# Optimization experiments

Measured on AMD Instinct MI355X. Metric: run time of the kernel, lower is better.

## Reference

```python
import jax, jax.numpy as jnp
import numpy as np

GROUP_SIZE = 128
EPS = 1e-6
# AWQ nibble interleave order within each int32
_AWQ_SHIFTS = jnp.array([0, 4, 1, 5, 2, 6, 3, 7], dtype=jnp.uint32) * 4


def dequant_awq(qw, qz, sc, group_size=GROUP_SIZE):
    # qw: (in, out//8) int32, qz: (in//g, out//8) int32, sc: (in//g, out) float
    in_dim = qw.shape[0]
    w4 = ((qw.astype(jnp.uint32)[:, :, None] >> _AWQ_SHIFTS) & 0xF).astype(sc.dtype)
    z4 = ((qz.astype(jnp.uint32)[:, :, None] >> _AWQ_SHIFTS) & 0xF).astype(sc.dtype)
    w4 = w4.reshape(in_dim, -1)                    # (in, out)
    z4 = z4.reshape(qz.shape[0], -1)               # (in//g, out)
    z = jnp.repeat(z4, group_size, axis=0)         # (in, out)
    s = jnp.repeat(sc, group_size, axis=0)         # (in, out)
    return (w4 - z) * s


def rmsnorm(x, w, eps=EPS):
    return x * w * jax.lax.rsqrt(jnp.mean(x * x, axis=-1, keepdims=True) + eps)


def setup_inputs() -> dict:
    key = jax.random.key(0)
    ks = jax.random.split(key, 16)
    H, I, G = 2048, 8192, GROUP_SIZE
    IMAX = 2**31 - 1
    d = {}
    d['x'] = jax.random.normal(ks[0], (2, 2048, H), dtype=jnp.float32)
    d['ln1_w'] = jnp.ones((H,), jnp.float32)
    d['ln2_w'] = jnp.ones((H,), jnp.float32)
    d['qkv_qw'] = jax.random.randint(ks[1], (H, 3 * H // 8), 0, IMAX, dtype=jnp.int32)
    d['qkv_qz'] = jax.random.randint(ks[2], (H // G, 3 * H // 8), 0, IMAX, dtype=jnp.int32)
    d['qkv_sc'] = jax.random.normal(ks[3], (H // G, 3 * H), dtype=jnp.float32) * 0.02
    d['o_qw'] = jax.random.randint(ks[4], (H, H // 8), 0, IMAX, dtype=jnp.int32)
    d['o_qz'] = jax.random.randint(ks[5], (H // G, H // 8), 0, IMAX, dtype=jnp.int32)
    d['o_sc'] = jax.random.normal(ks[6], (H // G, H), dtype=jnp.float32) * 0.02
    d['gu_qw'] = jax.random.randint(ks[7], (H, 2 * I // 8), 0, IMAX, dtype=jnp.int32)
    d['gu_qz'] = jax.random.randint(ks[8], (H // G, 2 * I // 8), 0, IMAX, dtype=jnp.int32)
    d['gu_sc'] = jax.random.normal(ks[9], (H // G, 2 * I), dtype=jnp.float32) * 0.02
    d['dn_qw'] = jax.random.randint(ks[10], (I, H // 8), 0, IMAX, dtype=jnp.int32)
    d['dn_qz'] = jax.random.randint(ks[11], (I // G, H // 8), 0, IMAX, dtype=jnp.int32)
    d['dn_sc'] = jax.random.normal(ks[12], (I // G, H), dtype=jnp.float32) * 0.02
    return d


def reference(x, ln1_w, ln2_w, qkv_qw, qkv_qz, qkv_sc, o_qw, o_qz, o_sc,
              gu_qw, gu_qz, gu_sc, dn_qw, dn_qz, dn_sc):
    H = x.shape[-1]
    # attention-ish block (mock: qkv proj, take q slice, o proj)
    residual = x
    h = rmsnorm(x, ln1_w)
    qkv = h @ dequant_awq(qkv_qw, qkv_qz, qkv_sc)          # (..., 3H)
    q = qkv[..., :H]
    o = q @ dequant_awq(o_qw, o_qz, o_sc)                  # (..., H)
    x = residual + o
    # SwiGLU MLP
    residual = x
    h = rmsnorm(x, ln2_w)
    gate_up = h @ dequant_awq(gu_qw, gu_qz, gu_sc)         # (..., 2I)
    gate, up = jnp.split(gate_up, 2, axis=-1)
    mlp = (jax.nn.silu(gate) * up) @ dequant_awq(dn_qw, dn_qz, dn_sc)
    return residual + mlp
```

## Files before the change

### kernel.cpp

```cpp
#include <hip/hip_runtime.h>
#include <hip/hip_bf16.h>
#include <stdint.h>

typedef __bf16 bf16x8 __attribute__((ext_vector_type(8)));
typedef __bf16 bf16x2 __attribute__((ext_vector_type(2)));
typedef float  f32x4  __attribute__((ext_vector_type(4)));

template <int V> struct ic { static constexpr int value = V; };

__device__ __forceinline__ void gload_lds16(const void* g, void* l) {
  __builtin_amdgcn_global_load_lds(
      (const __attribute__((address_space(1))) void*)g,
      (__attribute__((address_space(3))) void*)l, 16, 0, 0);
}

__global__ __launch_bounds__(256) void rmsnorm_kernel(
    const float* __restrict__ x, const float* __restrict__ w,
    __bf16* __restrict__ out) {
  constexpr int H = 2048;
  const int row = blockIdx.x;
  const int t = threadIdx.x;
  const float4* xr = (const float4*)(x + (size_t)row * H);
  float4 a = xr[t * 2 + 0];
  float4 b = xr[t * 2 + 1];
  float ss = a.x*a.x + a.y*a.y + a.z*a.z + a.w*a.w
           + b.x*b.x + b.y*b.y + b.z*b.z + b.w*b.w;
#pragma unroll
  for (int o = 32; o > 0; o >>= 1) ss += __shfl_xor(ss, o);
  __shared__ float red[4];
  if ((t & 63) == 0) red[t >> 6] = ss;
  __syncthreads();
  float tot = red[0] + red[1] + red[2] + red[3];
  float r = rsqrtf(tot * (1.0f / H) + 1e-6f);
  const float4* wr4 = (const float4*)w;
  float4 wa = wr4[t * 2 + 0];
  float4 wb = wr4[t * 2 + 1];
  bf16x8 ov;
  ov[0] = (__bf16)(a.x * wa.x * r);
  ov[1] = (__bf16)(a.y * wa.y * r);
  ov[2] = (__bf16)(a.z * wa.z * r);
  ov[3] = (__bf16)(a.w * wa.w * r);
  ov[4] = (__bf16)(b.x * wb.x * r);
  ov[5] = (__bf16)(b.y * wb.y * r);
  ov[6] = (__bf16)(b.z * wb.z * r);
  ov[7] = (__bf16)(b.w * wb.w * r);
  *(bf16x8*)(out + (size_t)row * H + (size_t)t * 8) = ov;
}

template <int GU>
__global__ __launch_bounds__(256) void dequant_t_kernel(
    const int* __restrict__ qw, const int* __restrict__ qz,
    const float* __restrict__ sc, __bf16* __restrict__ wt,
    int K, int Cp, int Nfull) {
  const int t = threadIdx.x;
  const int k0 = blockIdx.x * 128 + (t & 63) * 2;
  const int c0 = blockIdx.y * 64 + (t >> 6) * 16;
  const int g = k0 >> 7;
  const uint32_t* qw0 = (const uint32_t*)qw + (size_t)k0 * Cp + c0;
  const uint32_t* qw1 = qw0 + Cp;
  const uint32_t* qzr = (const uint32_t*)qz + (size_t)g * Cp + c0;
  const float* scr = sc + (size_t)g * Nfull + (size_t)c0 * 8;

  uint32_t u0[16], u1[16], z[16];
#pragma unroll
  for (int j = 0; j < 4; j++) {
    *(int4*)(&u0[j*4]) = *(const int4*)(qw0 + j*4);
    *(int4*)(&u1[j*4]) = *(const int4*)(qw1 + j*4);
    *(int4*)(&z[j*4])  = *(const int4*)(qzr + j*4);
  }

#pragma unroll
  for (int i = 0; i < 16; i++) {
#pragma unroll
    for (int s = 0; s < 8; s++) {
      const int sh = ((s >> 1) * 4) + ((s & 1) ? 16 : 0);
      const float zf = (float)((z[i] >> sh) & 15u);
      const float scv = scr[i * 8 + s];
      const float w0 = ((float)((u0[i] >> sh) & 15u) - zf) * scv;
      const float w1 = ((float)((u1[i] >> sh) & 15u) - zf) * scv;
      const int n = (c0 + i) * 8 + s;
      int row;
      if (GU) row = (n < 8192) ? ((n >> 4) * 32 + (n & 15))
                               : (((n - 8192) >> 4) * 32 + 16 + (n & 15));
      else    row = n;
      bf16x2 pv = {(__bf16)w0, (__bf16)w1};
      *(bf16x2*)(wt + (size_t)row * K + k0) = pv;
    }
  }
}

template <int BN, int EPI, int KC>
__global__ __launch_bounds__(512, 2) void gemm8p_kernel(
    const __bf16* __restrict__ A, const __bf16* __restrict__ Bt,
    void* __restrict__ Cv, const float* __restrict__ addend,
    int M, int N) {
  constexpr int NT = KC / 64;
  constexpr int BQ = BN / 64;
  constexpr int NSTRIP = BN / 4;
  constexpr int NI = NSTRIP / 16;

  __shared__ alignas(16) __bf16 As[8 * 4096];
  __shared__ alignas(16) __bf16 Bs[2 * BQ * 4096];

  const int t = threadIdx.x;
  const int w = t >> 6, l = t & 63;
  const int lm = l & 15, kb = l >> 4;
  const int l7 = lm & 7;
  const int wm = w >> 2, wn = w & 3;

  const size_t stat = (size_t)(t >> 3) * KC + (size_t)(((t & 7) ^ ((t >> 3) & 7)) << 3);

  const int nwg = gridDim.x;
  const int bid = blockIdx.x;
  const int swz = (bid & 7) * (nwg >> 3) + (bid >> 3);
  const int nbm = M >> 8;
  const int per_g = nbm * 8;
  const int grp = swz / per_g, v = swz % per_g;
  const int bm0 = (v % nbm) * 256;
  const int bn0 = (grp * 8 + v / nbm) * BN;

  const __bf16* Ab = A + (size_t)bm0 * KC;
  const __bf16* Bb = Bt + (size_t)bn0 * KC;

  const uint32_t gsw0 = (uint32_t)((kb ^ l7) << 4);
  const uint32_t gsw1 = (uint32_t)(((4 + kb) ^ l7) << 4);
  const uint32_t arow = (uint32_t)(wm * 16384 + lm * 128);
  const uint32_t aoff0 = arow + gsw0, aoff1 = arow + gsw1;
  const uint32_t brow = (BN == 256)
      ? (uint32_t)(wn * 8192 + lm * 128)
      : (uint32_t)((wn >> 1) * 8192 + (wn & 1) * 4096 + lm * 128);
  const uint32_t boff0 = brow + gsw0, boff1 = brow + gsw1;
  const char* AsC = (const char*)As;
  const char* BsC = (const char*)Bs;

  f32x4 acc[8][NI] = {};
  bf16x8 af[2][2][2];
  bf16x8 bfr[2][NI][2];

  auto ldAf = [&](int dD, int mi, bf16x8* dst) {
    const uint32_t imA = (uint32_t)((dD * 4 + (mi >> 2)) * 8192 + (mi & 3) * 2048);
    dst[0] = *(const bf16x8*)(AsC + aoff0 + imA);
    dst[1] = *(const bf16x8*)(AsC + aoff1 + imA);
  };
  auto ldBf = [&](int dD) {
#pragma unroll
    for (int ni = 0; ni < NI; ++ni) {
      const uint32_t imB = (uint32_t)(dD * BQ * 8192 + ni * 2048);
      bfr[dD][ni][0] = *(const bf16x8*)(BsC + boff0 + imB);
      bfr[dD][ni][1] = *(const bf16x8*)(BsC + boff1 + imB);
    }
  };
  auto mfma4 = [&](int q, bf16x8 afq[2][2], int dD) {
    __builtin_amdgcn_s_setprio(1);
#pragma unroll
    for (int kk = 0; kk < 2; ++kk)
#pragma unroll
      for (int ni = 0; ni < NI; ++ni)
#pragma unroll
        for (int m2 = 0; m2 < 2; ++m2)
          acc[q * 2 + m2][ni] = __builtin_amdgcn_mfma_f32_16x16x32_bf16(
              afq[m2][kk], bfr[dD][ni][kk], acc[q * 2 + m2][ni], 0, 0, 0);
    __builtin_amdgcn_s_setprio(0);
  };

#pragma unroll
  for (int qa = 0; qa < 4; ++qa)
    gload_lds16(Ab + stat + (size_t)(qa * 64) * KC, As + qa * 4096 + t * 8);
#pragma unroll
  for (int qb = 0; qb < BQ; ++qb)
    gload_lds16(Bb + stat + (size_t)(qb * 64) * KC, Bs + qb * 4096 + t * 8);
#pragma unroll
  for (int qb = 0; qb < BQ; ++qb)
    gload_lds16(Bb + stat + (size_t)(qb * 64) * KC + 64, Bs + (BQ + qb) * 4096 + t * 8);
  gload_lds16(Ab + stat + 64, As + 4 * 4096 + t * 8);
  gload_lds16(Ab + stat + (size_t)128 * KC + 64, As + 6 * 4096 + t * 8);
  if (BN == 256) asm volatile("s_waitcnt vmcnt(6)" ::: "memory");
  else           asm volatile("s_waitcnt vmcnt(4)" ::: "memory");
  __builtin_amdgcn_s_barrier();

  ldAf(0, 0, af[0][0]); ldAf(0, 1, af[0][1]);
  ldBf(0);
  asm volatile("" ::: "memory");

  const __bf16* pA0 = Ab + stat + 128;
  const __bf16* pA1 = Ab + stat + (size_t)64 * KC + 64;
  const __bf16* pA2 = Ab + stat + (size_t)128 * KC + 128;
  const __bf16* pA3 = Ab + stat + (size_t)192 * KC + 64;
  const __bf16* pB0 = Bb + stat + 128;
  const __bf16* pB1 = Bb + stat + (size_t)64 * KC + 128;
  const __bf16* pB2 = Bb + stat + (size_t)128 * KC + 128;
  const __bf16* pB3 = Bb + stat + (size_t)192 * KC + 128;

  auto tile = [&](auto Dc, auto Sc) {
    constexpr int D = decltype(Dc)::value;
    constexpr int STG = decltype(Sc)::value;
    ldAf(D, 2, af[1][0]); ldAf(D, 3, af[1][1]);
    asm volatile("" ::: "memory");
    if (STG >= 1) {
      gload_lds16(pA1, As + ((D ^ 1) * 4 + 1) * 4096 + t * 8);
      gload_lds16(pA3, As + ((D ^ 1) * 4 + 3) * 4096 + t * 8);
    }
    __builtin_amdgcn_s_barrier();
    mfma4(0, af[0], D);
    __builtin_amdgcn_s_barrier();
    ldAf(D, 4, af[0][0]); ldAf(D, 5, af[0][1]);
    asm volatile("" ::: "memory");
    if (STG == 2) {
      gload_lds16(pB0, Bs + (D * BQ + 0) * 4096 + t * 8);
      gload_lds16(pB1, Bs + (D * BQ + 1) * 4096 + t * 8);
    }
    __builtin_amdgcn_s_barrier();
    mfma4(1, af[1], D);
    __builtin_amdgcn_s_barrier();
    ldAf(D, 6, af[1][0]); ldAf(D, 7, af[1][1]);
    asm volatile("" ::: "memory");
    if (STG == 2) {
      if (BN == 256) {
        gload_lds16(pB2, Bs + (D * BQ + 2) * 4096 + t * 8);
        gload_lds16(pB3, Bs + (D * BQ + 3) * 4096 + t * 8);
      } else {
        gload_lds16(pA0, As + (D * 4 + 0) * 4096 + t * 8);
        gload_lds16(pA2, As + (D * 4 + 2) * 4096 + t * 8);
      }
    }
    __builtin_amdgcn_s_barrier();
    mfma4(2, af[0], D);
    __builtin_amdgcn_s_barrier();
    asm volatile("s_waitcnt lgkmcnt(0)" ::: "memory");
    __builtin_amdgcn_sched_barrier(0);
    if (STG == 2)      asm volatile("s_waitcnt vmcnt(4)" ::: "memory");
    else if (STG == 1) asm volatile("s_waitcnt vmcnt(0)" ::: "memory");
    __builtin_amdgcn_s_barrier();
    if (STG >= 1) {
      ldAf(D ^ 1, 0, af[0][0]); ldAf(D ^ 1, 1, af[0][1]);
      ldBf(D ^ 1);
      asm volatile("" ::: "memory");
    }
    if (STG == 2 && BN == 256) {
      gload_lds16(pA0, As + (D * 4 + 0) * 4096 + t * 8);
      gload_lds16(pA2, As + (D * 4 + 2) * 4096 + t * 8);
    }
    __builtin_amdgcn_sched_barrier(0);
    mfma4(3, af[1], D);
    __builtin_amdgcn_s_barrier();
    if (STG == 2) {
      pA0 += 64; pA1 += 64; pA2 += 64; pA3 += 64;
      pB0 += 64; pB1 += 64;
      if (BN == 256) { pB2 += 64; pB3 += 64; }
    }
  };

#pragma unroll 1
  for (int it = 0; it < NT / 2 - 1; ++it) {
    tile(ic<0>{}, ic<2>{});
    tile(ic<1>{}, ic<2>{});
  }
  tile(ic<0>{}, ic<1>{});
  tile(ic<1>{}, ic<0>{});

  const int crow0 = bm0 + wm * 128;
#pragma unroll
  for (int mi = 0; mi < 8; ++mi) {
    if (EPI == 2) {
#pragma unroll
      for (int p = 0; p < NI / 2; ++p) {
        const int ni = p * 2;
        const int col = ((bn0 + wn * 64 + ni * 16) >> 5) * 16 + lm;
#pragma unroll
        for (int r = 0; r < 4; ++r) {
          const int row = crow0 + mi * 16 + kb * 4 + r;
          const float gv = acc[mi][ni][r], uv = acc[mi][ni + 1][r];
          const float av = uv * (gv / (1.0f + __expf(-gv)));
          ((__bf16*)Cv)[(size_t)row * 8192 + col] = (__bf16)av;
        }
      }
    } else {
#pragma unroll
      for (int ni = 0; ni < NI; ++ni) {
        const int col = bn0 + wn * NSTRIP + ni * 16 + lm;
#pragma unroll
        for (int r = 0; r < 4; ++r) {
          const int row = crow0 + mi * 16 + kb * 4 + r;
          const size_t idx = (size_t)row * N + col;
          if (EPI == 0) ((__bf16*)Cv)[idx] = (__bf16)acc[mi][ni][r];
          else          ((float*)Cv)[idx] = addend[idx] + acc[mi][ni][r];
        }
      }
    }
  }
}

extern "C" void kernel_launch(void* const* d_in, const int* in_sizes, int n_in,
                              void* d_out, int out_size, void* d_ws, size_t ws_size,
                              hipStream_t stream) {
  const float* x      = (const float*)d_in[0];
  const float* ln1    = (const float*)d_in[1];
  const float* ln2    = (const float*)d_in[2];
  const int*   qkv_qw = (const int*)d_in[3];
  const int*   qkv_qz = (const int*)d_in[4];
  const float* qkv_sc = (const float*)d_in[5];
  const int*   o_qw   = (const int*)d_in[6];
  const int*   o_qz   = (const int*)d_in[7];
  const float* o_sc   = (const float*)d_in[8];
  const int*   gu_qw  = (const int*)d_in[9];
  const int*   gu_qz  = (const int*)d_in[10];
  const float* gu_sc  = (const float*)d_in[11];
  const int*   dn_qw  = (const int*)d_in[12];
  const int*   dn_qz  = (const int*)d_in[13];
  const float* dn_sc  = (const float*)d_in[14];

  constexpr int M = 4096;

  char* ws = (char*)d_ws;
  __bf16* h   = (__bf16*)(ws + 0);
  __bf16* q   = (__bf16*)(ws + 16777216ULL);
  float*  x2  = (float*)(ws + 33554432ULL);
  __bf16* W   = (__bf16*)(ws + 67108864ULL);
  __bf16* act = (__bf16*)(ws + 134217728ULL);
  __bf16* Wdn = (__bf16*)(ws + 0);

  rmsnorm_kernel<<<dim3(M), dim3(256), 0, stream>>>(x, ln1, h);
  dequant_t_kernel<0><<<dim3(16, 4), dim3(256), 0, stream>>>(qkv_qw, qkv_qz, qkv_sc, W, 2048, 768, 6144);
  gemm8p_kernel<128, 0, 2048><<<dim3(256), dim3(512), 0, stream>>>(h, W, (void*)q, nullptr, M, 2048);
  dequant_t_kernel<0><<<dim3(16, 4), dim3(256), 0, stream>>>(o_qw, o_qz, o_sc, W, 2048, 256, 2048);
  gemm8p_kernel<128, 1, 2048><<<dim3(256), dim3(512), 0, stream>>>(q, W, (void*)x2, x, M, 2048);
  rmsnorm_kernel<<<dim3(M), dim3(256), 0, stream>>>(x2, ln2, h);
  dequant_t_kernel<1><<<dim3(16, 32), dim3(256), 0, stream>>>(gu_qw, gu_qz, gu_sc, W, 2048, 2048, 16384);
  gemm8p_kernel<256, 2, 2048><<<dim3(1024), dim3(512), 0, stream>>>(h, W, (void*)act, nullptr, M, 16384);
  dequant_t_kernel<0><<<dim3(64, 4), dim3(256), 0, stream>>>(dn_qw, dn_qz, dn_sc, Wdn, 8192, 256, 2048);
  gemm8p_kernel<128, 1, 8192><<<dim3(256), dim3(512), 0, stream>>>(act, Wdn, d_out, x2, M, 2048);
}
```

Before: 513.4 us.

## Add 128x128-tile GEMM kernel for N=2048 projections to fill more CUs

Adds a new gemm128 kernel with 128x128 output tiles, a grouped block swizzle and a restructured LDS double-buffer pipeline. The qkv, o and down projections (N=2048) now use it with 512 blocks instead of 256. The goal is to fill all 256 CUs more evenly, where the larger tiles left them underoccupied. In exchange each block reuses A and B less and performs more global loads per FLOP. It also drops one compiler memory barrier in the existing gemm8p kernel.

Result: no change. 516.1 us (+0.5%).

```diff
diff --git a/kernel.cpp b/kernel.cpp
--- a/kernel.cpp
+++ b/kernel.cpp
@@ -234,7 +234,6 @@
     if (STG >= 1) {
       ldAf(D ^ 1, 0, af[0][0]); ldAf(D ^ 1, 1, af[0][1]);
       ldBf(D ^ 1);
-      asm volatile("" ::: "memory");
     }
     if (STG == 2 && BN == 256) {
       gload_lds16(pA0, As + (D * 4 + 0) * 4096 + t * 8);
@@ -285,6 +284,157 @@
           if (EPI == 0) ((__bf16*)Cv)[idx] = (__bf16)acc[mi][ni][r];
           else          ((float*)Cv)[idx] = addend[idx] + acc[mi][ni][r];
         }
+      }
+    }
+  }
+}
+
+template <int EPI, int KC>
+__global__ __launch_bounds__(512, 4) void gemm128_kernel(
+    const __bf16* __restrict__ A, const __bf16* __restrict__ Bt,
+    void* __restrict__ Cv, const float* __restrict__ addend,
+    int M, int N) {
+  constexpr int NT = KC / 64;
+
+  __shared__ alignas(16) __bf16 As[4 * 4096];
+  __shared__ alignas(16) __bf16 Bs[4 * 4096];
+
+  const int t = threadIdx.x;
+  const int w = t >> 6, l = t & 63;
+  const int lm = l & 15, kb = l >> 4;
+  const int l7 = lm & 7;
+  const int wm = w >> 2, wn = w & 3;
+
+  const size_t stat = (size_t)(t >> 3) * KC + (size_t)(((t & 7) ^ ((t >> 3) & 7)) << 3);
+
+  const int nwg = gridDim.x;
+  const int bid = blockIdx.x;
+  const int swz = (bid & 7) * (nwg >> 3) + (bid >> 3);
+  const int nbm = M >> 7;
+  const int per_g = nbm * 8;
+  const int grp = swz / per_g, v = swz % per_g;
+  const int bm0 = (v % nbm) * 128;
+  const int bn0 = (grp * 8 + v / nbm) * 128;
+
+  const __bf16* Ab = A + (size_t)bm0 * KC;
+  const __bf16* Bb = Bt + (size_t)bn0 * KC;
+
+  const uint32_t gsw0 = (uint32_t)((kb ^ l7) << 4);
+  const uint32_t gsw1 = (uint32_t)(((4 + kb) ^ l7) << 4);
+  const uint32_t aoff0 = (uint32_t)((wm * 32 + lm) * 128) + gsw0;
+  const uint32_t aoff1 = (uint32_t)((wm * 32 + lm) * 128) + gsw1;
+  const uint32_t bbase = (uint32_t)(((wn & 1) * 32 + lm) * 128 + (wn >> 1) * 8192);
+  const uint32_t boff0 = bbase + gsw0, boff1 = bbase + gsw1;
+  const char* AsC = (const char*)As;
+  const char* BsC = (const char*)Bs;
+
+  f32x4 acc[4][2] = {};
+  bf16x8 af[2][2];
+  bf16x8 bfr[2][2][2];
+
+  auto ldAf = [&](int dD, int mi) {
+    const uint32_t imA = (uint32_t)((dD * 2 + (mi >> 1)) * 8192 + (mi & 1) * 2048);
+    af[mi & 1][0] = *(const bf16x8*)(AsC + aoff0 + imA);
+    af[mi & 1][1] = *(const bf16x8*)(AsC + aoff1 + imA);
+  };
+  auto ldBf = [&](int dD) {
+#pragma unroll
+    for (int ni = 0; ni < 2; ++ni) {
+      const uint32_t imB = (uint32_t)(dD * 16384 + ni * 2048);
+      bfr[dD][ni][0] = *(const bf16x8*)(BsC + boff0 + imB);
+      bfr[dD][ni][1] = *(const bf16x8*)(BsC + boff1 + imB);
+    }
+  };
+  auto mfma1 = [&](int mi, int dD) {
+    __builtin_amdgcn_s_setprio(1);
+#pragma unroll
+    for (int kk = 0; kk < 2; ++kk)
+#pragma unroll
+      for (int ni = 0; ni < 2; ++ni)
+        acc[mi][ni] = __builtin_amdgcn_mfma_f32_16x16x32_bf16(
+            af[mi & 1][kk], bfr[dD][ni][kk], acc[mi][ni], 0, 0, 0);
+    __builtin_amdgcn_s_setprio(0);
+  };
+
+  gload_lds16(Ab + stat,                        As + 0 * 4096 + t * 8);
+  gload_lds16(Ab + stat + (size_t)64 * KC,      As + 1 * 4096 + t * 8);
+  gload_lds16(Bb + stat,                        Bs + 0 * 4096 + t * 8);
+  gload_lds16(Bb + stat + (size_t)64 * KC,      Bs + 1 * 4096 + t * 8);
+  gload_lds16(Bb + stat + 64,                   Bs + 2 * 4096 + t * 8);
+  gload_lds16(Bb + stat + (size_t)64 * KC + 64, Bs + 3 * 4096 + t * 8);
+  gload_lds16(Ab + stat + 64,                   As + 2 * 4096 + t * 8);
+  asm volatile("s_waitcnt vmcnt(3)" ::: "memory");
+  __builtin_amdgcn_s_barrier();
+
+  ldAf(0, 0);
+  ldBf(0);
+  asm volatile("" ::: "memory");
+
+  const __bf16* pAq1 = Ab + stat + (size_t)64 * KC + 64;
+  const __bf16* pAq0 = Ab + stat + 128;
+  const __bf16* pBq0 = Bb + stat + 128;
+  const __bf16* pBq1 = Bb + stat + (size_t)64 * KC + 128;
+
+  auto tile = [&](auto Dc, auto Sc) {
+    constexpr int D = decltype(Dc)::value;
+    constexpr int STG = decltype(Sc)::value;
+    ldAf(D, 1);
+    asm volatile("" ::: "memory");
+    if (STG >= 1)
+      gload_lds16(pAq1, As + ((D ^ 1) * 2 + 1) * 4096 + t * 8);
+    __builtin_amdgcn_s_barrier();
+    mfma1(0, D);
+    __builtin_amdgcn_s_barrier();
+    ldAf(D, 2);
+    asm volatile("" ::: "memory");
+    if (STG == 2) {
+      gload_lds16(pBq0, Bs + (D * 2 + 0) * 4096 + t * 8);
+      gload_lds16(pBq1, Bs + (D * 2 + 1) * 4096 + t * 8);
+    }
+    __builtin_amdgcn_s_barrier();
+    mfma1(1, D);
+    __builtin_amdgcn_s_barrier();
+    ldAf(D, 3);
+    asm volatile("" ::: "memory");
+    if (STG == 2)
+      gload_lds16(pAq0, As + (D * 2 + 0) * 4096 + t * 8);
+    __builtin_amdgcn_s_barrier();
+    mfma1(2, D);
+    __builtin_amdgcn_s_barrier();
+    asm volatile("s_waitcnt lgkmcnt(0)" ::: "memory");
+    __builtin_amdgcn_sched_barrier(0);
+    if (STG == 2)      asm volatile("s_waitcnt vmcnt(3)" ::: "memory");
+    else if (STG == 1) asm volatile("s_waitcnt vmcnt(0)" ::: "memory");
+    __builtin_amdgcn_s_barrier();
+    if (STG >= 1) {
+      ldAf(D ^ 1, 0);
+      ldBf(D ^ 1);
+    }
+    __builtin_amdgcn_sched_barrier(0);
+    mfma1(3, D);
+    __builtin_amdgcn_s_barrier();
+    if (STG == 2) { pAq0 += 64; pAq1 += 64; pBq0 += 64; pBq1 += 64; }
+  };
+
+#pragma unroll 1
+  for (int it = 0; it < NT / 2 - 1; ++it) {
+    tile(ic<0>{}, ic<2>{});
+    tile(ic<1>{}, ic<2>{});
+  }
+  tile(ic<0>{}, ic<1>{});
+  tile(ic<1>{}, ic<0>{});
+
+#pragma unroll
+  for (int mi = 0; mi < 4; ++mi) {
+#pragma unroll
+    for (int ni = 0; ni < 2; ++ni) {
+      const int col = bn0 + wn * 32 + ni * 16 + lm;
+#pragma unroll
+      for (int r = 0; r < 4; ++r) {
+        const int row = bm0 + (mi >> 1) * 64 + wm * 32 + (mi & 1) * 16 + kb * 4 + r;
+        const size_t idx = (size_t)row * N + col;
+        if (EPI == 0) ((__bf16*)Cv)[idx] = (__bf16)acc[mi][ni][r];
+        else          ((float*)Cv)[idx] = addend[idx] + acc[mi][ni][r];
       }
     }
   }
@@ -321,12 +471,12 @@
 
   rmsnorm_kernel<<<dim3(M), dim3(256), 0, stream>>>(x, ln1, h);
   dequant_t_kernel<0><<<dim3(16, 4), dim3(256), 0, stream>>>(qkv_qw, qkv_qz, qkv_sc, W, 2048, 768, 6144);
-  gemm8p_kernel<128, 0, 2048><<<dim3(256), dim3(512), 0, stream>>>(h, W, (void*)q, nullptr, M, 2048);
+  gemm128_kernel<0, 2048><<<dim3(512), dim3(512), 0, stream>>>(h, W, (void*)q, nullptr, M, 2048);
   dequant_t_kernel<0><<<dim3(16, 4), dim3(256), 0, stream>>>(o_qw, o_qz, o_sc, W, 2048, 256, 2048);
-  gemm8p_kernel<128, 1, 2048><<<dim3(256), dim3(512), 0, stream>>>(q, W, (void*)x2, x, M, 2048);
+  gemm128_kernel<1, 2048><<<dim3(512), dim3(512), 0, stream>>>(q, W, (void*)x2, x, M, 2048);
   rmsnorm_kernel<<<dim3(M), dim3(256), 0, stream>>>(x2, ln2, h);
   dequant_t_kernel<1><<<dim3(16, 32), dim3(256), 0, stream>>>(gu_qw, gu_qz, gu_sc, W, 2048, 2048, 16384);
   gemm8p_kernel<256, 2, 2048><<<dim3(1024), dim3(512), 0, stream>>>(h, W, (void*)act, nullptr, M, 16384);
   dequant_t_kernel<0><<<dim3(64, 4), dim3(256), 0, stream>>>(dn_qw, dn_qz, dn_sc, Wdn, 8192, 256, 2048);
-  gemm8p_kernel<128, 1, 8192><<<dim3(256), dim3(512), 0, stream>>>(act, Wdn, d_out, x2, M, 2048);
-}
+  gemm128_kernel<1, 8192><<<dim3(512), dim3(512), 0, stream>>>(act, Wdn, d_out, x2, M, 2048);
+}
```

## Split-K the down-projection GEMM with BN=256 and add a reduction kernel

Applied to the files above, without the earlier changes.

The down-projection GEMM (K=8192) now uses BN=256 tiles with K split into two slices of 4096, still launching 256 workgroups. Each slice writes fp32 partial sums to a workspace buffer, and a new reduce kernel adds both partials plus the residual into the output. The intent is a shorter serial K loop per workgroup and better per-tile reuse from the wider N tile. In exchange, the extra partial-buffer writes and reads, plus one more kernel launch, add memory traffic. One compiler memory fence after the fragment loads is also removed.

After: 596.0 us. 1.16x slower.

```diff
diff --git a/kernel.cpp b/kernel.cpp
--- a/kernel.cpp
+++ b/kernel.cpp
@@ -89,11 +89,11 @@
   }
 }
 
-template <int BN, int EPI, int KC>
+template <int BN, int EPI, int KC, int SPLITK>
 __global__ __launch_bounds__(512, 2) void gemm8p_kernel(
     const __bf16* __restrict__ A, const __bf16* __restrict__ Bt,
     void* __restrict__ Cv, const float* __restrict__ addend,
-    int M, int N) {
+    int M, int N, int ldk) {
   constexpr int NT = KC / 64;
   constexpr int BQ = BN / 64;
   constexpr int NSTRIP = BN / 4;
@@ -108,19 +108,30 @@
   const int l7 = lm & 7;
   const int wm = w >> 2, wn = w & 3;
 
-  const size_t stat = (size_t)(t >> 3) * KC + (size_t)(((t & 7) ^ ((t >> 3) & 7)) << 3);
+  const size_t stat = (size_t)(t >> 3) * ldk + (size_t)(((t & 7) ^ ((t >> 3) & 7)) << 3);
 
   const int nwg = gridDim.x;
   const int bid = blockIdx.x;
   const int swz = (bid & 7) * (nwg >> 3) + (bid >> 3);
   const int nbm = M >> 8;
-  const int per_g = nbm * 8;
-  const int grp = swz / per_g, v = swz % per_g;
-  const int bm0 = (v % nbm) * 256;
-  const int bn0 = (grp * 8 + v / nbm) * BN;
-
-  const __bf16* Ab = A + (size_t)bm0 * KC;
-  const __bf16* Bb = Bt + (size_t)bn0 * KC;
+  int bm0, bn0, slice;
+  if constexpr (SPLITK > 1) {
+    const int nbn = N / BN;
+    const int per_s = nbm * nbn;
+    slice = swz / per_s;
+    const int v2 = swz % per_s;
+    bm0 = (v2 % nbm) * 256;
+    bn0 = (v2 / nbm) * BN;
+  } else {
+    slice = 0;
+    const int per_g = nbm * 8;
+    const int grp = swz / per_g, v = swz % per_g;
+    bm0 = (v % nbm) * 256;
+    bn0 = (grp * 8 + v / nbm) * BN;
+  }
+
+  const __bf16* Ab = A + (size_t)bm0 * ldk + (size_t)slice * KC;
+  const __bf16* Bb = Bt + (size_t)bn0 * ldk + (size_t)slice * KC;
 
   const uint32_t gsw0 = (uint32_t)((kb ^ l7) << 4);
   const uint32_t gsw1 = (uint32_t)(((4 + kb) ^ l7) << 4);
@@ -165,15 +176,15 @@
 
 #pragma unroll
   for (int qa = 0; qa < 4; ++qa)
-    gload_lds16(Ab + stat + (size_t)(qa * 64) * KC, As + qa * 4096 + t * 8);
+    gload_lds16(Ab + stat + (size_t)(qa * 64) * ldk, As + qa * 4096 + t * 8);
 #pragma unroll
   for (int qb = 0; qb < BQ; ++qb)
-    gload_lds16(Bb + stat + (size_t)(qb * 64) * KC, Bs + qb * 4096 + t * 8);
+    gload_lds16(Bb + stat + (size_t)(qb * 64) * ldk, Bs + qb * 4096 + t * 8);
 #pragma unroll
   for (int qb = 0; qb < BQ; ++qb)
-    gload_lds16(Bb + stat + (size_t)(qb * 64) * KC + 64, Bs + (BQ + qb) * 4096 + t * 8);
+    gload_lds16(Bb + stat + (size_t)(qb * 64) * ldk + 64, Bs + (BQ + qb) * 4096 + t * 8);
   gload_lds16(Ab + stat + 64, As + 4 * 4096 + t * 8);
-  gload_lds16(Ab + stat + (size_t)128 * KC + 64, As + 6 * 4096 + t * 8);
+  gload_lds16(Ab + stat + (size_t)128 * ldk + 64, As + 6 * 4096 + t * 8);
   if (BN == 256) asm volatile("s_waitcnt vmcnt(6)" ::: "memory");
   else           asm volatile("s_waitcnt vmcnt(4)" ::: "memory");
   __builtin_amdgcn_s_barrier();
@@ -183,13 +194,13 @@
   asm volatile("" ::: "memory");
 
   const __bf16* pA0 = Ab + stat + 128;
-  const __bf16* pA1 = Ab + stat + (size_t)64 * KC + 64;
-  const __bf16* pA2 = Ab + stat + (size_t)128 * KC + 128;
-  const __bf16* pA3 = Ab + stat + (size_t)192 * KC + 64;
+  const __bf16* pA1 = Ab + stat + (size_t)64 * ldk + 64;
+  const __bf16* pA2 = Ab + stat + (size_t)128 * ldk + 128;
+  const __bf16* pA3 = Ab + stat + (size_t)192 * ldk + 64;
   const __bf16* pB0 = Bb + stat + 128;
-  const __bf16* pB1 = Bb + stat + (size_t)64 * KC + 128;
-  const __bf16* pB2 = Bb + stat + (size_t)128 * KC + 128;
-  const __bf16* pB3 = Bb + stat + (size_t)192 * KC + 128;
+  const __bf16* pB1 = Bb + stat + (size_t)64 * ldk + 128;
+  const __bf16* pB2 = Bb + stat + (size_t)128 * ldk + 128;
+  const __bf16* pB3 = Bb + stat + (size_t)192 * ldk + 128;
 
   auto tile = [&](auto Dc, auto Sc) {
     constexpr int D = decltype(Dc)::value;
@@ -234,7 +245,6 @@
     if (STG >= 1) {
       ldAf(D ^ 1, 0, af[0][0]); ldAf(D ^ 1, 1, af[0][1]);
       ldBf(D ^ 1);
-      asm volatile("" ::: "memory");
     }
     if (STG == 2 && BN == 256) {
       gload_lds16(pA0, As + (D * 4 + 0) * 4096 + t * 8);
@@ -259,6 +269,7 @@
   tile(ic<1>{}, ic<0>{});
 
   const int crow0 = bm0 + wm * 128;
+  float* Cout = (float*)Cv + (size_t)slice * M * N;
 #pragma unroll
   for (int mi = 0; mi < 8; ++mi) {
     if (EPI == 2) {
@@ -282,12 +293,28 @@
         for (int r = 0; r < 4; ++r) {
           const int row = crow0 + mi * 16 + kb * 4 + r;
           const size_t idx = (size_t)row * N + col;
-          if (EPI == 0) ((__bf16*)Cv)[idx] = (__bf16)acc[mi][ni][r];
-          else          ((float*)Cv)[idx] = addend[idx] + acc[mi][ni][r];
+          if (EPI == 0)      ((__bf16*)Cv)[idx] = (__bf16)acc[mi][ni][r];
+          else if (EPI == 1) ((float*)Cv)[idx] = addend[idx] + acc[mi][ni][r];
+          else               Cout[idx] = acc[mi][ni][r];
         }
       }
     }
   }
+}
+
+__global__ __launch_bounds__(256) void reduce_kernel(
+    const float* __restrict__ x2, const float* __restrict__ p0,
+    const float* __restrict__ p1, float* __restrict__ out) {
+  const size_t i = ((size_t)blockIdx.x * 256 + threadIdx.x) * 4;
+  const float4 a = *(const float4*)(x2 + i);
+  const float4 b = *(const float4*)(p0 + i);
+  const float4 c = *(const float4*)(p1 + i);
+  float4 o;
+  o.x = a.x + b.x + c.x;
+  o.y = a.y + b.y + c.y;
+  o.z = a.z + b.z + c.z;
+  o.w = a.w + b.w + c.w;
+  *(float4*)(out + i) = o;
 }
 
 extern "C" void kernel_launch(void* const* d_in, const int* in_sizes, int n_in,
@@ -312,21 +339,23 @@
   constexpr int M = 4096;
 
   char* ws = (char*)d_ws;
-  __bf16* h   = (__bf16*)(ws + 0);
-  __bf16* q   = (__bf16*)(ws + 16777216ULL);
-  float*  x2  = (float*)(ws + 33554432ULL);
-  __bf16* W   = (__bf16*)(ws + 67108864ULL);
-  __bf16* act = (__bf16*)(ws + 134217728ULL);
-  __bf16* Wdn = (__bf16*)(ws + 0);
+  __bf16* h    = (__bf16*)(ws + 0);
+  __bf16* q    = (__bf16*)(ws + 16777216ULL);
+  float*  x2   = (float*)(ws + 33554432ULL);
+  __bf16* W    = (__bf16*)(ws + 67108864ULL);
+  __bf16* act  = (__bf16*)(ws + 134217728ULL);
+  __bf16* Wdn  = (__bf16*)(ws + 0);
+  float*  part = (float*)(ws + 201326592ULL);
 
   rmsnorm_kernel<<<dim3(M), dim3(256), 0, stream>>>(x, ln1, h);
   dequant_t_kernel<0><<<dim3(16, 4), dim3(256), 0, stream>>>(qkv_qw, qkv_qz, qkv_sc, W, 2048, 768, 6144);
-  gemm8p_kernel<128, 0, 2048><<<dim3(256), dim3(512), 0, stream>>>(h, W, (void*)q, nullptr, M, 2048);
+  gemm8p_kernel<128, 0, 2048, 1><<<dim3(256), dim3(512), 0, stream>>>(h, W, (void*)q, nullptr, M, 2048, 2048);
   dequant_t_kernel<0><<<dim3(16, 4), dim3(256), 0, stream>>>(o_qw, o_qz, o_sc, W, 2048, 256, 2048);
-  gemm8p_kernel<128, 1, 2048><<<dim3(256), dim3(512), 0, stream>>>(q, W, (void*)x2, x, M, 2048);
+  gemm8p_kernel<128, 1, 2048, 1><<<dim3(256), dim3(512), 0, stream>>>(q, W, (void*)x2, x, M, 2048, 2048);
   rmsnorm_kernel<<<dim3(M), dim3(256), 0, stream>>>(x2, ln2, h);
   dequant_t_kernel<1><<<dim3(16, 32), dim3(256), 0, stream>>>(gu_qw, gu_qz, gu_sc, W, 2048, 2048, 16384);
-  gemm8p_kernel<256, 2, 2048><<<dim3(1024), dim3(512), 0, stream>>>(h, W, (void*)act, nullptr, M, 16384);
+  gemm8p_kernel<256, 2, 2048, 1><<<dim3(1024), dim3(512), 0, stream>>>(h, W, (void*)act, nullptr, M, 16384, 2048);
   dequant_t_kernel<0><<<dim3(64, 4), dim3(256), 0, stream>>>(dn_qw, dn_qz, dn_sc, Wdn, 8192, 256, 2048);
-  gemm8p_kernel<128, 1, 8192><<<dim3(256), dim3(512), 0, stream>>>(act, Wdn, d_out, x2, M, 2048);
-}
+  gemm8p_kernel<256, 3, 4096, 2><<<dim3(256), dim3(512), 0, stream>>>(act, Wdn, (void*)part, nullptr, M, 2048, 8192);
+  reduce_kernel<<<dim3(8192), dim3(256), 0, stream>>>(x2, part, part + (size_t)M * 2048, (float*)d_out);
+}
```
